# Kernel tuning notes

Hardware: AMD Instinct MI355X
Metric: run time of the kernel (lower is better)

## Reference

```python
import jax, jax.numpy as jnp
import numpy as np

HID = 512
HEADS = 8
HD = HID // HEADS  # 64


def setup_inputs() -> dict:
    key = jax.random.key(0)
    ks = jax.random.split(key, 16)
    B, LQ, LK = 2, 384, 384
    s_in = 1.0 / np.sqrt(HID)
    s_hd = 1.0 / np.sqrt(HD)
    return {
        "query": jax.random.normal(ks[0], (B, LQ, HID), jnp.float32),
        "key":   jax.random.normal(ks[1], (B, LK, HID), jnp.float32),
        "value": jax.random.normal(ks[2], (B, LK, HID), jnp.float32),
        # linear weights stored as (in, out) so y = x @ W + b
        "Wq": jax.random.uniform(ks[3], (HID, HID), jnp.float32, -s_in, s_in),
        "bq": jnp.zeros((HID,), jnp.float32),
        "Wk": jax.random.uniform(ks[4], (HID, HID), jnp.float32, -s_in, s_in),
        "bk": jnp.zeros((HID,), jnp.float32),
        "Wv": jax.random.uniform(ks[5], (HID, HID), jnp.float32, -s_in, s_in),
        "bv": jnp.zeros((HID,), jnp.float32),
        "Ww": jax.random.uniform(ks[6], (HD, HD), jnp.float32, -s_hd, s_hd),
        "bw": jnp.zeros((HD,), jnp.float32),
        "Wu": jax.random.uniform(ks[7], (HD, HD), jnp.float32, -s_hd, s_hd),
        "bu": jnp.zeros((HD,), jnp.float32),
        "vv": jax.random.uniform(ks[8], (HD,), jnp.float32, -s_hd, s_hd),
        "Wo": jax.random.uniform(ks[9], (HID, HID), jnp.float32, -s_in, s_in),
        "bo": jnp.zeros((HID,), jnp.float32),
    }


def reference(query, key, value, Wq, bq, Wk, bk, Wv, bv, Ww, bw, Wu, bu, vv, Wo, bo):
    B, LQ, _ = query.shape
    LK = key.shape[1]
    scale = jnp.sqrt(jnp.asarray(HD, query.dtype))

    def split_heads(x, L):
        return x.reshape(B, L, HEADS, HD).transpose(0, 2, 1, 3)  # [B,H,L,hd]

    Q = split_heads(query @ Wq + bq, LQ)
    K = split_heads(key @ Wk + bk, LK)
    V = split_heads(value @ Wv + bv, LK)

    qW = Q @ Ww + bw            # [B,H,Lq,hd]
    kU = K @ Wu + bu            # [B,H,Lk,hd]
    # additive energy: tanh(W(Q)+U(K)) . vv  -> [B,H,Lq,Lk]
    e = jnp.tanh(qW[:, :, :, None, :] + kU[:, :, None, :, :])  # [B,H,Lq,Lk,hd]
    energy = jnp.einsum('bhqkd,d->bhqk', e, vv) / scale

    attention = jax.nn.softmax(energy, axis=-1)
    x = jnp.einsum('bhqk,bhkd->bhqd', attention, V)
    x = x.transpose(0, 2, 1, 3).reshape(B, LQ, HID)
    x = x @ Wo + bo
    return (x, attention)
```

## Files before the change

kernel.cpp:

```cpp
#include <hip/hip_runtime.h>

#define HID 512
#define HEADS 8
#define HD 64
#define BATCH 2
#define SEQ 384
#define MROWS (BATCH * SEQ)
#define KT_N 48
#define APACK_S8 (48 * KT_N * 64)
#define BPACK_S8 (32 * KT_N * 64)

#define C1 2.8853900817779268f
#define SSCL 0.18033688011112043f

typedef __attribute__((ext_vector_type(8))) short s8v;
typedef __attribute__((ext_vector_type(4))) float f4v;

__device__ __forceinline__ unsigned short bf16_rne(float x) {
    union { float f; unsigned u; } v; v.f = x;
    unsigned r = v.u + 0x7FFFu + ((v.u >> 16) & 1u);
    return (unsigned short)(r >> 16);
}
__device__ __forceinline__ float bf16_val(unsigned short h) {
    union { float f; unsigned u; } v; v.u = ((unsigned)h) << 16; return v.f;
}

__device__ __forceinline__ void pack_a_one(const float* __restrict__ src,
                                           s8v* __restrict__ dst, int rem)
{
    int g = rem & 63, m = rem >> 6;
    const float4* sp = (const float4*)(src + (size_t)m * HID + g * 8);
    float4 v0 = sp[0], v1 = sp[1];
    float vals[8] = {v0.x, v0.y, v0.z, v0.w, v1.x, v1.y, v1.z, v1.w};
    s8v hi, lo;
    #pragma unroll
    for (int j = 0; j < 8; ++j) {
        unsigned short h = bf16_rne(vals[j]);
        hi[j] = (short)h;
        lo[j] = (short)bf16_rne(vals[j] - bf16_val(h));
    }
    int mt = m >> 4, kt = g >> 2;
    int lanei = (m & 15) | ((g & 3) << 4);
    size_t base = ((size_t)mt * KT_N) * 64 + lanei;
    dst[base + (size_t)kt * 64]        = hi;
    dst[base + (size_t)(16 + kt) * 64] = hi;
    dst[base + (size_t)(32 + kt) * 64] = lo;
}

__global__ __launch_bounds__(256) void prep_pack_kernel(
    const float* __restrict__ Wq, const float* __restrict__ bq,
    const float* __restrict__ Wk, const float* __restrict__ bk,
    const float* __restrict__ Ww, const float* __restrict__ bw,
    const float* __restrict__ Wu, const float* __restrict__ bu,
    const float* __restrict__ vv,
    float* __restrict__ wqe, float* __restrict__ wke,
    float* __restrict__ bqe, float* __restrict__ bke,
    float* __restrict__ vv2,
    const float* __restrict__ q, const float* __restrict__ k, const float* __restrict__ v,
    s8v* __restrict__ Aq, s8v* __restrict__ Ak, s8v* __restrict__ Av)
{
    if (blockIdx.x >= 2053) {
        int bx = blockIdx.x - 2053;
        int p = bx / 192;
        int rem = (bx % 192) * 256 + threadIdx.x;
        const float* src = (p == 0) ? q : (p == 1) ? k : v;
        s8v* dst = (p == 0) ? Aq : (p == 1) ? Ak : Av;
        pack_a_one(src, dst, rem);
        return;
    }
    int tid = blockIdx.x * 256 + threadIdx.x;
    if (tid < 262144) {
        int i = tid >> 9, n = tid & 511, h = n >> 6, j = n & 63;
        const float* wrow = Wq + i * HID + h * HD;
        float s = 0.f;
        #pragma unroll 8
        for (int t = 0; t < 64; ++t) s = fmaf(wrow[t], Ww[t * 64 + j], s);
        wqe[tid] = s;
    } else if (tid < 524288) {
        int idx = tid - 262144;
        int i = idx >> 9, n = idx & 511, h = n >> 6, j = n & 63;
        const float* wrow = Wk + i * HID + h * HD;
        float s = 0.f;
        #pragma unroll 8
        for (int t = 0; t < 64; ++t) s = fmaf(wrow[t], Wu[t * 64 + j], s);
        wke[idx] = s;
    } else if (tid < 524800) {
        int n = tid - 524288, h = n >> 6, j = n & 63;
        float s = bw[j];
        for (int t = 0; t < 64; ++t) s = fmaf(bq[h * 64 + t], Ww[t * 64 + j], s);
        bqe[n] = s;
    } else if (tid < 525312) {
        int n = tid - 524800, h = n >> 6, j = n & 63;
        float s = bu[j];
        for (int t = 0; t < 64; ++t) s = fmaf(bk[h * 64 + t], Wu[t * 64 + j], s);
        bke[n] = s;
    } else if (tid < 525376) {
        int d = tid - 525312;
        vv2[d] = -2.0f * vv[d];
    }
}

__global__ __launch_bounds__(256) void pack_a1_kernel(
    const float* __restrict__ x, s8v* __restrict__ Ax)
{
    pack_a_one(x, Ax, blockIdx.x * 256 + threadIdx.x);
}

__device__ __forceinline__ void pack_w_one(const float* __restrict__ W,
                                           s8v* __restrict__ dst, int rem)
{
    int kg = rem >> 9, n = rem & 511;
    s8v hi, lo;
    #pragma unroll
    for (int j = 0; j < 8; ++j) {
        float x = W[(size_t)(kg * 8 + j) * HID + n];
        unsigned short h = bf16_rne(x);
        hi[j] = (short)h;
        lo[j] = (short)bf16_rne(x - bf16_val(h));
    }
    int nt = n >> 4, kt = kg >> 2;
    int lanei = (n & 15) | ((kg & 3) << 4);
    size_t base = ((size_t)nt * KT_N) * 64 + lanei;
    dst[base + (size_t)kt * 64]        = hi;
    dst[base + (size_t)(16 + kt) * 64] = lo;
    dst[base + (size_t)(32 + kt) * 64] = hi;
}

__global__ __launch_bounds__(256) void pack_w_kernel(
    const float* __restrict__ w0, const float* __restrict__ w1,
    const float* __restrict__ w2, const float* __restrict__ w3,
    s8v* __restrict__ B0, s8v* __restrict__ B1,
    s8v* __restrict__ B2, s8v* __restrict__ B3)
{
    int bx = blockIdx.x;
    int p = bx >> 7;
    int rem = (bx & 127) * 256 + threadIdx.x;
    const float* W = (p == 0) ? w0 : (p == 1) ? w1 : (p == 2) ? w2 : w3;
    s8v* dst = (p == 0) ? B0 : (p == 1) ? B1 : (p == 2) ? B2 : B3;
    pack_w_one(W, dst, rem);
}

template <int MODE>
__device__ __forceinline__ void mfma_gemm_body(
    const s8v* __restrict__ Ap, const s8v* __restrict__ Bp,
    const float* __restrict__ bias, float* __restrict__ out,
    int mt0, int nt0)
{
    int lane = threadIdx.x & 63;

    const s8v* a0p = Ap + (size_t)(mt0 * KT_N) * 64 + lane;
    const s8v* a1p = a0p + (size_t)KT_N * 64;
    const s8v* b0p = Bp + (size_t)(nt0 * KT_N) * 64 + lane;
    const s8v* b1p = b0p + (size_t)KT_N * 64;

    f4v acc00 = {0.f, 0.f, 0.f, 0.f};
    f4v acc01 = {0.f, 0.f, 0.f, 0.f};
    f4v acc10 = {0.f, 0.f, 0.f, 0.f};
    f4v acc11 = {0.f, 0.f, 0.f, 0.f};

    s8v xa0 = a0p[0], xa1 = a1p[0], xb0 = b0p[0], xb1 = b1p[0];
    #pragma unroll 1
    for (int kt = 0; kt < KT_N; kt += 2) {
        int o1 = (kt + 1) * 64;
        s8v ya0 = a0p[o1], ya1 = a1p[o1], yb0 = b0p[o1], yb1 = b1p[o1];
        acc00 = __builtin_amdgcn_mfma_f32_16x16x32_bf16(xa0, xb0, acc00, 0, 0, 0);
        acc01 = __builtin_amdgcn_mfma_f32_16x16x32_bf16(xa0, xb1, acc01, 0, 0, 0);
        acc10 = __builtin_amdgcn_mfma_f32_16x16x32_bf16(xa1, xb0, acc10, 0, 0, 0);
        acc11 = __builtin_amdgcn_mfma_f32_16x16x32_bf16(xa1, xb1, acc11, 0, 0, 0);
        int o2 = (kt + 2 < KT_N) ? (kt + 2) * 64 : 0;
        xa0 = a0p[o2]; xa1 = a1p[o2]; xb0 = b0p[o2]; xb1 = b1p[o2];
        acc00 = __builtin_amdgcn_mfma_f32_16x16x32_bf16(ya0, yb0, acc00, 0, 0, 0);
        acc01 = __builtin_amdgcn_mfma_f32_16x16x32_bf16(ya0, yb1, acc01, 0, 0, 0);
        acc10 = __builtin_amdgcn_mfma_f32_16x16x32_bf16(ya1, yb0, acc10, 0, 0, 0);
        acc11 = __builtin_amdgcn_mfma_f32_16x16x32_bf16(ya1, yb1, acc11, 0, 0, 0);
    }

    int quad = lane >> 4, c16 = lane & 15;
    int col0 = nt0 * 16 + c16, col1 = col0 + 16;
    float bias0 = bias[col0], bias1 = bias[col1];
    int row0 = mt0 * 16 + quad * 4;
    int row1 = row0 + 16;

    #pragma unroll
    for (int r = 0; r < 4; ++r) {
        float y;
        #define WR(ROW, COL, Y)                                                     \
        {                                                                           \
            float yy = (Y);                                                         \
            if (MODE != 0) yy = __builtin_amdgcn_exp2f(C1 * yy);                    \
            if (MODE == 2) {                                                        \
                int b2 = (ROW) / SEQ, kk = (ROW) - b2 * SEQ;                        \
                int hh = (COL) >> 6, dd = (COL) & 63;                               \
                out[(((size_t)((b2 * 8 + hh) * 16 + (dd >> 2)) * SEQ + kk) << 2)    \
                    + (dd & 3)] = yy;                                               \
            } else {                                                                \
                out[(size_t)(ROW) * HID + (COL)] = yy;                              \
            }                                                                       \
        }
        y = acc00[r] + bias0; WR(row0 + r, col0, y);
        y = acc01[r] + bias1; WR(row0 + r, col1, y);
        y = acc10[r] + bias0; WR(row1 + r, col0, y);
        y = acc11[r] + bias1; WR(row1 + r, col1, y);
        #undef WR
    }
}

__global__ __launch_bounds__(64) void proj3_mfma_kernel(
    const s8v* __restrict__ Aq, const s8v* __restrict__ Ak, const s8v* __restrict__ Av,
    const s8v* __restrict__ Bq, const s8v* __restrict__ Bk, const s8v* __restrict__ Bv,
    const float* __restrict__ bqe, const float* __restrict__ bke, const float* __restrict__ bv,
    float* __restrict__ Eq, float* __restrict__ Ek4, float* __restrict__ V)
{
    int p = blockIdx.z;
    int mt0 = blockIdx.x * 2, nt0 = blockIdx.y * 2;
    if (p == 0)      mfma_gemm_body<1>(Aq, Bq, bqe, Eq,  mt0, nt0);
    else if (p == 1) mfma_gemm_body<2>(Ak, Bk, bke, Ek4, mt0, nt0);
    else             mfma_gemm_body<0>(Av, Bv, bv,  V,   mt0, nt0);
}

__global__ __launch_bounds__(64) void out_mfma_kernel(
    const s8v* __restrict__ Ax, const s8v* __restrict__ Bo,
    const float* __restrict__ bo, float* __restrict__ out)
{
    mfma_gemm_body<0>(Ax, Bo, bo, out, blockIdx.x * 2, blockIdx.y * 2);
}

__global__ __launch_bounds__(256, 4) void attn_kernel(
    const float* __restrict__ Eq, const float* __restrict__ Ek4,
    const float* __restrict__ V, const float* __restrict__ vv2,
    float* __restrict__ attnOut, float* __restrict__ X)
{
    __shared__ float2 aP[4][SEQ];

    int bh = blockIdx.y;
    int b = bh >> 3, h = bh & 7;
    int tid = threadIdx.x;
    int wave = __builtin_amdgcn_readfirstlane(tid >> 6);
    int lane = tid & 63;
    int q0 = blockIdx.x * 8 + wave * 2, q1 = q0 + 1;

    const float* eq0 = Eq + (size_t)(b * SEQ + q0) * HID + h * HD;
    const float* eq1 = eq0 + HID;
    const float4* ekbase = (const float4*)Ek4 + (size_t)bh * 16 * SEQ + lane;

    float e0[6], e1[6];
    #pragma unroll
    for (int t = 0; t < 6; ++t) { e0[t] = 0.f; e1[t] = 0.f; }

    #pragma unroll 1
    for (int c = 0; c < 4; ++c) {
        float g0[16], g1[16], w[16];
        #pragma unroll
        for (int j = 0; j < 16; ++j) {
            g0[j] = eq0[c * 16 + j];
            g1[j] = eq1[c * 16 + j];
            w[j]  = vv2[c * 16 + j];
        }
        const float4* ekc = ekbase + (size_t)c * 4 * SEQ;
        float4 k0 = ekc[0 * SEQ], k1 = ekc[1 * SEQ];
        float4 k2 = ekc[2 * SEQ], k3 = ekc[3 * SEQ];
        #pragma unroll
        for (int kt = 0; kt < 6; ++kt) {
            float4 n0, n1, n2, n3;
            if (kt < 5) {
                const float4* np = ekc + (kt + 1) * 64;
                n0 = np[0 * SEQ]; n1 = np[1 * SEQ];
                n2 = np[2 * SEQ]; n3 = np[3 * SEQ];
            }
            float r0 = e0[kt], r1 = e1[kt];
            #define EN(J, KV)                                                      \
            {                                                                      \
                float t0 = __builtin_amdgcn_rcpf(fmaf(g0[J], (KV), 1.f));          \
                float t1 = __builtin_amdgcn_rcpf(fmaf(g1[J], (KV), 1.f));          \
                r0 = fmaf(w[J], t0, r0);                                           \
                r1 = fmaf(w[J], t1, r1);                                           \
            }
            EN(0,  k0.x) EN(1,  k0.y) EN(2,  k0.z) EN(3,  k0.w)
            EN(4,  k1.x) EN(5,  k1.y) EN(6,  k1.z) EN(7,  k1.w)
            EN(8,  k2.x) EN(9,  k2.y) EN(10, k2.z) EN(11, k2.w)
            EN(12, k3.x) EN(13, k3.y) EN(14, k3.z) EN(15, k3.w)
            #undef EN
            e0[kt] = r0; e1[kt] = r1;
            k0 = n0; k1 = n1; k2 = n2; k3 = n3;
        }
    }

    float m0 = e0[0], m1 = e1[0];
    #pragma unroll
    for (int t = 1; t < 6; ++t) { m0 = fmaxf(m0, e0[t]); m1 = fmaxf(m1, e1[t]); }
    #pragma unroll
    for (int off = 1; off < 64; off <<= 1) {
        m0 = fmaxf(m0, __shfl_xor(m0, off));
        m1 = fmaxf(m1, __shfl_xor(m1, off));
    }
    float a0[6], a1[6], s0 = 0.f, s1 = 0.f;
    #pragma unroll
    for (int t = 0; t < 6; ++t) {
        a0[t] = __builtin_amdgcn_exp2f((e0[t] - m0) * SSCL); s0 += a0[t];
        a1[t] = __builtin_amdgcn_exp2f((e1[t] - m1) * SSCL); s1 += a1[t];
    }
    #pragma unroll
    for (int off = 1; off < 64; off <<= 1) {
        s0 += __shfl_xor(s0, off);
        s1 += __shfl_xor(s1, off);
    }
    float z0 = __builtin_amdgcn_rcpf(s0), z1 = __builtin_amdgcn_rcpf(s1);

    size_t abase = (size_t)bh * SEQ * SEQ + (size_t)q0 * SEQ;
    #pragma unroll
    for (int t = 0; t < 6; ++t) {
        float v0 = a0[t] * z0, v1 = a1[t] * z1;
        attnOut[abase + t * 64 + lane] = v0;
        attnOut[abase + SEQ + t * 64 + lane] = v1;
        aP[wave][t * 64 + lane] = make_float2(v0, v1);
    }

    int ko = lane >> 4, d4p = lane & 15;
    const float4* vb = (const float4*)&V[(size_t)b * SEQ * HID + h * HD + d4p * 4];
    float4 x0 = make_float4(0.f, 0.f, 0.f, 0.f);
    float4 x1 = make_float4(0.f, 0.f, 0.f, 0.f);
    #pragma unroll 8
    for (int k = ko; k < SEQ; k += 4) {
        float4 v = vb[(size_t)k * (HID / 4)];
        float2 a = aP[wave][k];
        x0.x = fmaf(a.x, v.x, x0.x); x0.y = fmaf(a.x, v.y, x0.y);
        x0.z = fmaf(a.x, v.z, x0.z); x0.w = fmaf(a.x, v.w, x0.w);
        x1.x = fmaf(a.y, v.x, x1.x); x1.y = fmaf(a.y, v.y, x1.y);
        x1.z = fmaf(a.y, v.z, x1.z); x1.w = fmaf(a.y, v.w, x1.w);
    }
    #pragma unroll
    for (int off = 16; off < 64; off <<= 1) {
        x0.x += __shfl_xor(x0.x, off); x0.y += __shfl_xor(x0.y, off);
        x0.z += __shfl_xor(x0.z, off); x0.w += __shfl_xor(x0.w, off);
        x1.x += __shfl_xor(x1.x, off); x1.y += __shfl_xor(x1.y, off);
        x1.z += __shfl_xor(x1.z, off); x1.w += __shfl_xor(x1.w, off);
    }
    if (ko == 0) {
        *(float4*)&X[(size_t)(b * SEQ + q0) * HID + h * HD + d4p * 4] = x0;
        *(float4*)&X[(size_t)(b * SEQ + q1) * HID + h * HD + d4p * 4] = x1;
    }
}

extern "C" void kernel_launch(void* const* d_in, const int* in_sizes, int n_in,
                              void* d_out, int out_size, void* d_ws, size_t ws_size,
                              hipStream_t stream)
{
    const float* query = (const float*)d_in[0];
    const float* key   = (const float*)d_in[1];
    const float* value = (const float*)d_in[2];
    const float* Wq = (const float*)d_in[3];
    const float* bq = (const float*)d_in[4];
    const float* Wk = (const float*)d_in[5];
    const float* bk = (const float*)d_in[6];
    const float* Wv = (const float*)d_in[7];
    const float* bv = (const float*)d_in[8];
    const float* Ww = (const float*)d_in[9];
    const float* bw = (const float*)d_in[10];
    const float* Wu = (const float*)d_in[11];
    const float* bu = (const float*)d_in[12];
    const float* vv = (const float*)d_in[13];
    const float* Wo = (const float*)d_in[14];
    const float* bo = (const float*)d_in[15];

    float* out_x    = (float*)d_out;
    float* out_attn = out_x + (size_t)MROWS * HID;

    float* ws  = (float*)d_ws;
    float* wqe = ws;
    float* wke = wqe + 262144;
    float* bqe = wke + 262144;
    float* bke = bqe + 512;
    float* vv2 = bke + 512;
    float* EqB = vv2 + 64;
    float* Ek4 = EqB + 393216;
    float* Vw  = Ek4 + 393216;
    float* Xw  = Vw + 393216;

    s8v* packs = (s8v*)(Xw + 393216);
    s8v* Aq = packs;
    s8v* Ak = Aq + APACK_S8;
    s8v* Av = Ak + APACK_S8;
    s8v* Ax = Av + APACK_S8;
    s8v* Bq = Ax + APACK_S8;
    s8v* Bk = Bq + BPACK_S8;
    s8v* Bv = Bk + BPACK_S8;
    s8v* Bo = Bv + BPACK_S8;

    prep_pack_kernel<<<dim3(2629), 256, 0, stream>>>(
        Wq, bq, Wk, bk, Ww, bw, Wu, bu, vv,
        wqe, wke, bqe, bke, vv2,
        query, key, value, Aq, Ak, Av);
    pack_w_kernel<<<dim3(512), 256, 0, stream>>>(wqe, wke, Wv, Wo, Bq, Bk, Bv, Bo);
    proj3_mfma_kernel<<<dim3(24, 16, 3), 64, 0, stream>>>(Aq, Ak, Av, Bq, Bk, Bv,
                                                          bqe, bke, bv,
                                                          EqB, Ek4, Vw);
    attn_kernel<<<dim3(48, 16), 256, 0, stream>>>(EqB, Ek4, Vw, vv2, out_attn, Xw);
    pack_a1_kernel<<<dim3(192), 256, 0, stream>>>(Xw, Ax);
    out_mfma_kernel<<<dim3(24, 16), 64, 0, stream>>>(Ax, Bo, bo, out_x);
}
```

Baseline: 154.2 us.

## Fuse prep and weight-pack kernels; pack attention output directly into MFMA layout

Merges the weight-folding, bias-folding, input packing and weight packing into a single launch. The Wq·Ww and Wk·Wu products are now computed inside the packer and written straight to bf16 hi/lo split form, so the fp32 intermediates no longer go through global memory. The attention kernel now writes its output directly in the packed split-bf16 A layout, which removes the separate pack_a1 launch and the X round trip. This drops two launches and some memory traffic, but the fused packer does redundant loads of Wsmall and is branch-heterogeneous across blocks.

```diff
diff --git a/kernel.cpp b/kernel.cpp
--- a/kernel.cpp
+++ b/kernel.cpp
@@ -47,76 +47,15 @@
     dst[base + (size_t)(32 + kt) * 64] = lo;
 }
 
-__global__ __launch_bounds__(256) void prep_pack_kernel(
-    const float* __restrict__ Wq, const float* __restrict__ bq,
-    const float* __restrict__ Wk, const float* __restrict__ bk,
-    const float* __restrict__ Ww, const float* __restrict__ bw,
-    const float* __restrict__ Wu, const float* __restrict__ bu,
-    const float* __restrict__ vv,
-    float* __restrict__ wqe, float* __restrict__ wke,
-    float* __restrict__ bqe, float* __restrict__ bke,
-    float* __restrict__ vv2,
-    const float* __restrict__ q, const float* __restrict__ k, const float* __restrict__ v,
-    s8v* __restrict__ Aq, s8v* __restrict__ Ak, s8v* __restrict__ Av)
-{
-    if (blockIdx.x >= 2053) {
-        int bx = blockIdx.x - 2053;
-        int p = bx / 192;
-        int rem = (bx % 192) * 256 + threadIdx.x;
-        const float* src = (p == 0) ? q : (p == 1) ? k : v;
-        s8v* dst = (p == 0) ? Aq : (p == 1) ? Ak : Av;
-        pack_a_one(src, dst, rem);
-        return;
-    }
-    int tid = blockIdx.x * 256 + threadIdx.x;
-    if (tid < 262144) {
-        int i = tid >> 9, n = tid & 511, h = n >> 6, j = n & 63;
-        const float* wrow = Wq + i * HID + h * HD;
-        float s = 0.f;
-        #pragma unroll 8
-        for (int t = 0; t < 64; ++t) s = fmaf(wrow[t], Ww[t * 64 + j], s);
-        wqe[tid] = s;
-    } else if (tid < 524288) {
-        int idx = tid - 262144;
-        int i = idx >> 9, n = idx & 511, h = n >> 6, j = n & 63;
-        const float* wrow = Wk + i * HID + h * HD;
-        float s = 0.f;
-        #pragma unroll 8
-        for (int t = 0; t < 64; ++t) s = fmaf(wrow[t], Wu[t * 64 + j], s);
-        wke[idx] = s;
-    } else if (tid < 524800) {
-        int n = tid - 524288, h = n >> 6, j = n & 63;
-        float s = bw[j];
-        for (int t = 0; t < 64; ++t) s = fmaf(bq[h * 64 + t], Ww[t * 64 + j], s);
-        bqe[n] = s;
-    } else if (tid < 525312) {
-        int n = tid - 524800, h = n >> 6, j = n & 63;
-        float s = bu[j];
-        for (int t = 0; t < 64; ++t) s = fmaf(bk[h * 64 + t], Wu[t * 64 + j], s);
-        bke[n] = s;
-    } else if (tid < 525376) {
-        int d = tid - 525312;
-        vv2[d] = -2.0f * vv[d];
-    }
-}
-
-__global__ __launch_bounds__(256) void pack_a1_kernel(
-    const float* __restrict__ x, s8v* __restrict__ Ax)
-{
-    pack_a_one(x, Ax, blockIdx.x * 256 + threadIdx.x);
-}
-
-__device__ __forceinline__ void pack_w_one(const float* __restrict__ W,
-                                           s8v* __restrict__ dst, int rem)
-{
-    int kg = rem >> 9, n = rem & 511;
+__device__ __forceinline__ void pack_w_store(s8v* __restrict__ dst,
+                                             const float vals[8], int kg, int n)
+{
     s8v hi, lo;
     #pragma unroll
     for (int j = 0; j < 8; ++j) {
-        float x = W[(size_t)(kg * 8 + j) * HID + n];
-        unsigned short h = bf16_rne(x);
+        unsigned short h = bf16_rne(vals[j]);
         hi[j] = (short)h;
-        lo[j] = (short)bf16_rne(x - bf16_val(h));
+        lo[j] = (short)bf16_rne(vals[j] - bf16_val(h));
     }
     int nt = n >> 4, kt = kg >> 2;
     int lanei = (n & 15) | ((kg & 3) << 4);
@@ -126,18 +65,81 @@
     dst[base + (size_t)(32 + kt) * 64] = hi;
 }
 
-__global__ __launch_bounds__(256) void pack_w_kernel(
-    const float* __restrict__ w0, const float* __restrict__ w1,
-    const float* __restrict__ w2, const float* __restrict__ w3,
-    s8v* __restrict__ B0, s8v* __restrict__ B1,
-    s8v* __restrict__ B2, s8v* __restrict__ B3)
-{
-    int bx = blockIdx.x;
-    int p = bx >> 7;
-    int rem = (bx & 127) * 256 + threadIdx.x;
-    const float* W = (p == 0) ? w0 : (p == 1) ? w1 : (p == 2) ? w2 : w3;
-    s8v* dst = (p == 0) ? B0 : (p == 1) ? B1 : (p == 2) ? B2 : B3;
-    pack_w_one(W, dst, rem);
+__device__ __forceinline__ void pack_w_one(const float* __restrict__ W,
+                                           s8v* __restrict__ dst, int rem)
+{
+    int kg = rem >> 9, n = rem & 511;
+    float vals[8];
+    #pragma unroll
+    for (int j = 0; j < 8; ++j)
+        vals[j] = W[(size_t)(kg * 8 + j) * HID + n];
+    pack_w_store(dst, vals, kg, n);
+}
+
+__device__ __forceinline__ void fold_pack_w_one(const float* __restrict__ Wbig,
+                                                const float* __restrict__ Wsmall,
+                                                s8v* __restrict__ dst, int rem)
+{
+    int kg = __builtin_amdgcn_readfirstlane(rem >> 9);
+    int n  = rem & 511;
+    int h  = __builtin_amdgcn_readfirstlane(n >> 6);
+    int d  = n & 63;
+    const float* wr = Wbig + (size_t)(kg * 8) * HID + h * HD;
+    float acc[8] = {0.f, 0.f, 0.f, 0.f, 0.f, 0.f, 0.f, 0.f};
+    #pragma unroll 8
+    for (int t = 0; t < 64; ++t) {
+        float wv = Wsmall[t * 64 + d];
+        #pragma unroll
+        for (int j = 0; j < 8; ++j)
+            acc[j] = fmaf(wr[(size_t)j * HID + t], wv, acc[j]);
+    }
+    pack_w_store(dst, acc, kg, n);
+}
+
+__global__ __launch_bounds__(256) void pack_all_kernel(
+    const float* __restrict__ q, const float* __restrict__ k, const float* __restrict__ v,
+    const float* __restrict__ Wq, const float* __restrict__ bq,
+    const float* __restrict__ Wk, const float* __restrict__ bk,
+    const float* __restrict__ Wv, const float* __restrict__ Wo,
+    const float* __restrict__ Ww, const float* __restrict__ bw,
+    const float* __restrict__ Wu, const float* __restrict__ bu,
+    const float* __restrict__ vv,
+    s8v* __restrict__ Aq, s8v* __restrict__ Ak, s8v* __restrict__ Av,
+    s8v* __restrict__ Bq, s8v* __restrict__ Bk, s8v* __restrict__ Bv, s8v* __restrict__ Bo,
+    float* __restrict__ bqe, float* __restrict__ bke, float* __restrict__ vv2)
+{
+    int bx = blockIdx.x, tid = threadIdx.x;
+    if (bx < 576) {
+        int p = bx / 192;
+        int rem = (bx % 192) * 256 + tid;
+        const float* src = (p == 0) ? q : (p == 1) ? k : v;
+        s8v* dst = (p == 0) ? Aq : (p == 1) ? Ak : Av;
+        pack_a_one(src, dst, rem);
+    } else if (bx < 704) {
+        pack_w_one(Wv, Bv, (bx - 576) * 256 + tid);
+    } else if (bx < 832) {
+        pack_w_one(Wo, Bo, (bx - 704) * 256 + tid);
+    } else if (bx < 960) {
+        fold_pack_w_one(Wq, Ww, Bq, (bx - 832) * 256 + tid);
+    } else if (bx < 1088) {
+        fold_pack_w_one(Wk, Wu, Bk, (bx - 960) * 256 + tid);
+    } else {
+        for (int i = tid; i < 1088; i += 256) {
+            if (i < 512) {
+                int h = i >> 6, j = i & 63;
+                float s = bw[j];
+                for (int t = 0; t < 64; ++t) s = fmaf(bq[h * 64 + t], Ww[t * 64 + j], s);
+                bqe[i] = s;
+            } else if (i < 1024) {
+                int n = i - 512, h = n >> 6, j = n & 63;
+                float s = bu[j];
+                for (int t = 0; t < 64; ++t) s = fmaf(bk[h * 64 + t], Wu[t * 64 + j], s);
+                bke[n] = s;
+            } else {
+                vv2[i - 1024] = -2.0f * vv[i - 1024];
+            }
+        }
+    }
 }
 
 template <int MODE>
@@ -228,7 +230,7 @@
 __global__ __launch_bounds__(256, 4) void attn_kernel(
     const float* __restrict__ Eq, const float* __restrict__ Ek4,
     const float* __restrict__ V, const float* __restrict__ vv2,
-    float* __restrict__ attnOut, float* __restrict__ X)
+    float* __restrict__ attnOut, s8v* __restrict__ Ax)
 {
     __shared__ float2 aP[4][SEQ];
 
@@ -335,9 +337,38 @@
         x1.x += __shfl_xor(x1.x, off); x1.y += __shfl_xor(x1.y, off);
         x1.z += __shfl_xor(x1.z, off); x1.w += __shfl_xor(x1.w, off);
     }
+
     if (ko == 0) {
-        *(float4*)&X[(size_t)(b * SEQ + q0) * HID + h * HD + d4p * 4] = x0;
-        *(float4*)&X[(size_t)(b * SEQ + q1) * HID + h * HD + d4p * 4] = x1;
+        float4 p0, p1;
+        p0.x = __shfl_xor(x0.x, 1); p0.y = __shfl_xor(x0.y, 1);
+        p0.z = __shfl_xor(x0.z, 1); p0.w = __shfl_xor(x0.w, 1);
+        p1.x = __shfl_xor(x1.x, 1); p1.y = __shfl_xor(x1.y, 1);
+        p1.z = __shfl_xor(x1.z, 1); p1.w = __shfl_xor(x1.w, 1);
+        float vals[8];
+        int row;
+        if ((lane & 1) == 0) {
+            vals[0] = x0.x; vals[1] = x0.y; vals[2] = x0.z; vals[3] = x0.w;
+            vals[4] = p0.x; vals[5] = p0.y; vals[6] = p0.z; vals[7] = p0.w;
+            row = b * SEQ + q0;
+        } else {
+            vals[0] = p1.x; vals[1] = p1.y; vals[2] = p1.z; vals[3] = p1.w;
+            vals[4] = x1.x; vals[5] = x1.y; vals[6] = x1.z; vals[7] = x1.w;
+            row = b * SEQ + q1;
+        }
+        int g = h * 8 + (lane >> 1);
+        s8v hi, lo;
+        #pragma unroll
+        for (int j = 0; j < 8; ++j) {
+            unsigned short hh = bf16_rne(vals[j]);
+            hi[j] = (short)hh;
+            lo[j] = (short)bf16_rne(vals[j] - bf16_val(hh));
+        }
+        int mt = row >> 4, kt2 = g >> 2;
+        int lanei = (row & 15) | ((g & 3) << 4);
+        size_t base = ((size_t)mt * KT_N) * 64 + lanei;
+        Ax[base + (size_t)kt2 * 64]        = hi;
+        Ax[base + (size_t)(16 + kt2) * 64] = hi;
+        Ax[base + (size_t)(32 + kt2) * 64] = lo;
     }
 }
 
@@ -366,17 +397,14 @@
     float* out_attn = out_x + (size_t)MROWS * HID;
 
     float* ws  = (float*)d_ws;
-    float* wqe = ws;
-    float* wke = wqe + 262144;
-    float* bqe = wke + 262144;
+    float* bqe = ws;
     float* bke = bqe + 512;
     float* vv2 = bke + 512;
     float* EqB = vv2 + 64;
     float* Ek4 = EqB + 393216;
     float* Vw  = Ek4 + 393216;
-    float* Xw  = Vw + 393216;
-
-    s8v* packs = (s8v*)(Xw + 393216);
+
+    s8v* packs = (s8v*)(Vw + 393216);
     s8v* Aq = packs;
     s8v* Ak = Aq + APACK_S8;
     s8v* Av = Ak + APACK_S8;
@@ -386,15 +414,14 @@
     s8v* Bv = Bk + BPACK_S8;
     s8v* Bo = Bv + BPACK_S8;
 
-    prep_pack_kernel<<<dim3(2629), 256, 0, stream>>>(
-        Wq, bq, Wk, bk, Ww, bw, Wu, bu, vv,
-        wqe, wke, bqe, bke, vv2,
-        query, key, value, Aq, Ak, Av);
-    pack_w_kernel<<<dim3(512), 256, 0, stream>>>(wqe, wke, Wv, Wo, Bq, Bk, Bv, Bo);
+    pack_all_kernel<<<dim3(1089), 256, 0, stream>>>(
+        query, key, value,
+        Wq, bq, Wk, bk, Wv, Wo, Ww, bw, Wu, bu, vv,
+        Aq, Ak, Av, Bq, Bk, Bv, Bo,
+        bqe, bke, vv2);
     proj3_mfma_kernel<<<dim3(24, 16, 3), 64, 0, stream>>>(Aq, Ak, Av, Bq, Bk, Bv,
                                                           bqe, bke, bv,
                                                           EqB, Ek4, Vw);
-    attn_kernel<<<dim3(48, 16), 256, 0, stream>>>(EqB, Ek4, Vw, vv2, out_attn, Xw);
-    pack_a1_kernel<<<dim3(192), 256, 0, stream>>>(Xw, Ax);
+    attn_kernel<<<dim3(48, 16), 256, 0, stream>>>(EqB, Ek4, Vw, vv2, out_attn, Ax);
     out_mfma_kernel<<<dim3(24, 16), 64, 0, stream>>>(Ax, Bo, bo, out_x);
 }
```

Result: faster. 148.0 us (-4.0%).
